# Kernel optimization log

Measured on AMD Instinct MI355X. Metric: run time of the kernel, lower is better.

Reference implementation:

```python
import jax, jax.numpy as jnp
import numpy as np
from jax import lax

INV_SQRT2 = np.float32(1.0 / np.sqrt(2.0))

def conv2d(x, w, b=None, stride=1, pad=0):
    y = lax.conv_general_dilated(x, w, (stride, stride), [(pad, pad), (pad, pad)],
                                 dimension_numbers=('NCHW', 'OIHW', 'NCHW'))
    return y if b is None else y + b[None, :, None, None]

def haar_dwt2_zero(x):
    # pytorch_wavelets DWTForward(J=1, wave='haar', mode='zero') for odd H,W:
    # pad one zero at the end of each spatial dim, then pairwise Haar analysis.
    x = jnp.pad(x, ((0, 0), (0, 0), (0, 1), (0, 1)))
    xe, xo = x[..., 0::2], x[..., 1::2]
    lo_w, hi_w = (xe + xo) * INV_SQRT2, (xe - xo) * INV_SQRT2
    def rows(t):
        te, to = t[:, :, 0::2, :], t[:, :, 1::2, :]
        return (te + to) * INV_SQRT2, (te - to) * INV_SQRT2
    ll, lh = rows(lo_w)
    hl, hh = rows(hi_w)
    return ll, lh, hl, hh  # cA, cH, cV, cD

def pixel_shuffle2(x):
    B, C, H, W = x.shape
    co = C // 4
    return x.reshape(B, co, 2, 2, H, W).transpose(0, 1, 4, 2, 5, 3).reshape(B, co, H * 2, W * 2)

def gaussian_kernel5(sigma=0.5):
    r = np.arange(5, dtype=np.float64) - 2.0
    k = np.exp(-(r ** 2) / (2.0 * sigma * sigma))
    return jnp.asarray((k / k.sum()).astype(np.float32))

_GK = gaussian_kernel5(0.5)

def gaussian_blur5(x4d):
    # cv2.GaussianBlur ksize=(5,5) sigma=0.5, default BORDER_REFLECT_101 -> 'reflect' pad
    p = jnp.pad(x4d, ((0, 0), (0, 0), (2, 2), (2, 2)), mode='reflect')
    p = conv2d(p, _GK.reshape(1, 1, 5, 1))
    return conv2d(p, _GK.reshape(1, 1, 1, 5))

def channel_attention(x, w1, w2):
    avg = jnp.mean(x, axis=(2, 3), keepdims=True)
    mx = jnp.max(x, axis=(2, 3), keepdims=True)
    mlp = lambda v: conv2d(jax.nn.relu(conv2d(v, w1)), w2)
    return jax.nn.sigmoid(mlp(avg) + mlp(mx)) * x

def _forward(x, w_x1, b_x1, w_x2, b_x2, w_x3, b_x3, w_hi, b_hi, w_lo, b_lo,
             ca1_w1, ca1_w2, ca2_w1, ca2_w2, w_cat, b_cat, w_c9a, b_c9a, w_c9b, b_c9b):
    f1 = jax.nn.relu(conv2d(x, w_x1, b_x1))            # (1,16,H,W)
    f2 = jax.nn.relu(conv2d(f1, w_x2, b_x2))           # (1,8,H,W)
    tmp12 = jax.nn.relu(conv2d(f2, w_x3, b_x3))        # (1,1,H,W)
    cA, cH, cV, cD = haar_dwt2_zero(tmp12)             # each (1,1,(H+1)/2,(W+1)/2)
    hf = pixel_shuffle2(jax.nn.relu(conv2d(jnp.concatenate([cH, cV, cD], 1), w_hi, b_hi, pad=1)))
    lf = pixel_shuffle2(jax.nn.relu(conv2d(cA, w_lo, b_lo, pad=1)))  # (1,1,H+5,W+5)
    # original detaches hf (cpu->numpy->cv2->cuda): gradients do not flow through it
    hf = gaussian_blur5(lax.stop_gradient(hf))
    hf = channel_attention(hf, ca1_w1, ca1_w2)
    lf = channel_attention(lf, ca2_w1, ca2_w2)
    alpha = 1.0
    cat = jax.nn.relu(conv2d(jnp.concatenate([alpha * hf, (1.0 - alpha) * lf], 1), w_cat, b_cat))
    f12 = tmp12 + cat                                   # (1,1,H,W)
    h = jax.nn.relu(conv2d(f12, w_c9a, b_c9a, pad=1))   # (1,32,H,W)
    return jax.nn.relu(conv2d(h, w_c9b, b_c9b, pad=1))  # (1,64,H,W)

def setup_inputs() -> dict:
    key = jax.random.key(0)
    ks = jax.random.split(key, 24)
    f32 = jnp.float32
    n = lambda k, s, sc=0.05: jax.random.normal(k, s, f32) * sc
    H = W = 511
    return {
        'x': jax.random.normal(ks[0], (1, 204, H, W), f32),
        'w_x1': n(ks[1], (16, 204, 1, 1)), 'b_x1': n(ks[2], (16,)),
        'w_x2': n(ks[3], (8, 16, 1, 1)),   'b_x2': n(ks[4], (8,)),
        'w_x3': n(ks[5], (1, 8, 1, 1)),    'b_x3': n(ks[6], (1,)),
        'w_hi': n(ks[7], (4, 3, 1, 1)),    'b_hi': n(ks[8], (4,)),
        'w_lo': n(ks[9], (4, 1, 1, 1)),    'b_lo': n(ks[10], (4,)),
        'ca1_w1': n(ks[11], (1, 1, 1, 1), 0.5), 'ca1_w2': n(ks[12], (1, 1, 1, 1), 0.5),
        'ca2_w1': n(ks[13], (1, 1, 1, 1), 0.5), 'ca2_w2': n(ks[14], (1, 1, 1, 1), 0.5),
        'w_cat': n(ks[15], (1, 2, 6, 6)),  'b_cat': n(ks[16], (1,)),
        'w_c9a': n(ks[17], (32, 1, 3, 3)), 'b_c9a': n(ks[18], (32,)),
        'w_c9b': n(ks[19], (64, 32, 3, 3)), 'b_c9b': n(ks[20], (64,)),
    }

def reference(x, w_x1, b_x1, w_x2, b_x2, w_x3, b_x3, w_hi, b_hi, w_lo, b_lo,
              ca1_w1, ca1_w2, ca2_w1, ca2_w2, w_cat, b_cat, w_c9a, b_c9a, w_c9b, b_c9b):
    return _forward(x, w_x1, b_x1, w_x2, b_x2, w_x3, b_x3, w_hi, b_hi, w_lo, b_lo,
                    ca1_w1, ca1_w2, ca2_w1, ca2_w2, w_cat, b_cat, w_c9a, b_c9a, w_c9b, b_c9b)
```

## Files before the change

kernel.cpp:

```cpp
#include <hip/hip_runtime.h>
#include <hip/hip_bf16.h>
#include <math.h>

#define NP    261121
#define WPX   520
#define ROWN  4160
#define PSTR  2138240
#define NBLUR 1041

typedef __attribute__((ext_vector_type(8))) short short8;
typedef __attribute__((ext_vector_type(4))) float f32x4;
typedef __attribute__((ext_vector_type(4), aligned(4))) float f32x4a;

static __device__ __forceinline__ unsigned short f2bf(float f) {
    unsigned int u = __builtin_bit_cast(unsigned int, f);
    u += 0x7FFFu + ((u >> 16) & 1u);
    return (unsigned short)(u >> 16);
}

static __device__ __forceinline__ short bf16s(float f) {
    __hip_bfloat16 h = __float2bfloat16(f);
    return __builtin_bit_cast(short, h);
}

__global__ __launch_bounds__(256, 4) void k_conv123(const float* __restrict__ x,
                                                    const float* __restrict__ w_x1,
                                                    const float* __restrict__ b1,
                                                    const float* __restrict__ w2,
                                                    const float* __restrict__ b2,
                                                    const float* __restrict__ w3,
                                                    const float* __restrict__ b3,
                                                    float* __restrict__ tmp12)
{
    int lane = threadIdx.x & 63, wave = threadIdx.x >> 6;
    int lpx = lane & 15, kg = lane >> 4;
    int s = blockIdx.x * 4 + wave;
    int pxb = s * 64;
    if (pxb > NP - 64) pxb = NP - 64;

    short8 afr[7];
    {
        const float* wrow = w_x1 + lpx * 204;
#pragma unroll
        for (int ks = 0; ks < 7; ++ks)
#pragma unroll
            for (int j = 0; j < 8; ++j) {
                int c = ks * 32 + kg * 8 + j;
                afr[ks][j] = (short)f2bf(c < 204 ? wrow[c] : 0.f);
            }
    }

    const float* pj[8];
#pragma unroll
    for (int j = 0; j < 8; ++j)
        pj[j] = x + (size_t)(kg * 8 + j) * NP + pxb + lpx * 4;

    f32x4 acc[4];
#pragma unroll
    for (int n = 0; n < 4; ++n) acc[n] = (f32x4){0.f, 0.f, 0.f, 0.f};

    f32x4a qA[8], qB[8];

#define LOADKS(Q, KS) do { \
        _Pragma("unroll") \
        for (int j = 0; j < 8; ++j) { \
            const size_t o = ((KS) < 6 || kg * 8 + j < 12) ? (size_t)(KS) * 32 * NP : 0; \
            Q[j] = *reinterpret_cast<const f32x4a*>(pj[j] + o); \
        } \
    } while (0)

#define PROC(Q, KS) do { \
        short8 bfr[4]; \
        _Pragma("unroll") \
        for (int n = 0; n < 4; ++n) \
            _Pragma("unroll") \
            for (int j = 0; j < 8; ++j) \
                bfr[n][j] = bf16s(Q[j][n]); \
        _Pragma("unroll") \
        for (int n = 0; n < 4; ++n) \
            acc[n] = __builtin_amdgcn_mfma_f32_16x16x32_bf16(afr[KS], bfr[n], acc[n], 0, 0, 0); \
    } while (0)

    LOADKS(qA, 0);
    LOADKS(qB, 1);
    PROC(qA, 0);
    LOADKS(qA, 2);
    PROC(qB, 1);
    LOADKS(qB, 3);
    PROC(qA, 2);
    LOADKS(qA, 4);
    PROC(qB, 3);
    LOADKS(qB, 5);
    PROC(qA, 4);
    LOADKS(qA, 6);
    PROC(qB, 5);
    PROC(qA, 6);
#undef LOADKS
#undef PROC

    float4 b1v = *reinterpret_cast<const float4*>(b1 + kg * 4);
    float4 w2v[8];
#pragma unroll
    for (int j = 0; j < 8; ++j)
        w2v[j] = *reinterpret_cast<const float4*>(w2 + j * 16 + kg * 4);
    float b2v[8], w3v[8];
#pragma unroll
    for (int j = 0; j < 8; ++j) { b2v[j] = b2[j]; w3v[j] = w3[j]; }
    float b3v = b3[0];

    f32x4 resv;
#pragma unroll
    for (int n = 0; n < 4; ++n) {
        float f0 = fmaxf(acc[n][0] + b1v.x, 0.f);
        float f1 = fmaxf(acc[n][1] + b1v.y, 0.f);
        float f2 = fmaxf(acc[n][2] + b1v.z, 0.f);
        float f3 = fmaxf(acc[n][3] + b1v.w, 0.f);
        float tmp = b3v;
#pragma unroll
        for (int j = 0; j < 8; ++j) {
            float sj = f0 * w2v[j].x;
            sj = fmaf(f1, w2v[j].y, sj);
            sj = fmaf(f2, w2v[j].z, sj);
            sj = fmaf(f3, w2v[j].w, sj);
            sj += __shfl_xor(sj, 16, 64);
            sj += __shfl_xor(sj, 32, 64);
            tmp = fmaf(fmaxf(sj + b2v[j], 0.f), w3v[j], tmp);
        }
        resv[n] = fmaxf(tmp, 0.f);
    }
    if (kg == 0)
        *reinterpret_cast<f32x4a*>(tmp12 + pxb + lpx * 4) = resv;
}

__global__ __launch_bounds__(256) void k_dwt(const float* __restrict__ tmp12,
                                             const float* __restrict__ w_hi,
                                             const float* __restrict__ b_hi,
                                             const float* __restrict__ w_c9b,
                                             float* __restrict__ hf,
                                             unsigned short* __restrict__ wb2,
                                             unsigned short* __restrict__ h2)
{
    int t = blockIdx.x * 256 + threadIdx.x;

    if (t < 18432) {
        int o = t / 288, ck = t - o * 288;
        int c = ck / 9, k = ck - c * 9;
        wb2[k * 2048 + o * 32 + c] = f2bf(w_c9b[t]);
    }
    short8 z8 = {0, 0, 0, 0, 0, 0, 0, 0};
    if (t < 4160) {
        int pl = t / 1040;
        int rr = t - pl * 1040;
        int row = rr >= 520 ? 512 : 0;
        int ch  = rr >= 520 ? rr - 520 : rr;
        *reinterpret_cast<short8*>(h2 + (size_t)pl * PSTR + (size_t)row * ROWN + ch * 8) = z8;
    }
    int z = t - 4160;
    if (z >= 0 && z < 6132) {
        int row = z / 12 + 1;
        int j = z - (row - 1) * 12;
        int pl = j / 3, cidx = j - pl * 3;
        int col = (cidx == 0) ? 0 : (cidx == 1 ? 512 : 513);
        *reinterpret_cast<short8*>(h2 + (size_t)pl * PSTR + (size_t)row * ROWN + col * 8) = z8;
    }

    const float INV = 0.70710678118654752440f;
    if (t >= 258 * 258) return;
    int h = t / 258, w = t - h * 258;

    float wh[12], bh[4];
#pragma unroll
    for (int i = 0; i < 12; ++i) wh[i] = w_hi[i];
#pragma unroll
    for (int o = 0; o < 4; ++o) bh[o] = b_hi[o];

    float v[4];
    if (h == 0 || h == 257 || w == 0 || w == 257) {
#pragma unroll
        for (int o = 0; o < 4; ++o) v[o] = fmaxf(bh[o], 0.f);
    } else {
        int hh = h - 1, ww = w - 1;
        int r0 = 2 * hh, r1 = 2 * hh + 1, c0 = 2 * ww, c1 = 2 * ww + 1;
        float a = tmp12[r0 * 511 + c0];
        float b = (c1 < 511) ? tmp12[r0 * 511 + c1] : 0.f;
        float c = (r1 < 511) ? tmp12[r1 * 511 + c0] : 0.f;
        float d = (r1 < 511 && c1 < 511) ? tmp12[r1 * 511 + c1] : 0.f;
        float lo0 = (a + b) * INV, hi0 = (a - b) * INV;
        float lo1 = (c + d) * INV, hi1 = (c - d) * INV;
        float cH = (lo0 - lo1) * INV;
        float cV = (hi0 + hi1) * INV;
        float cD = (hi0 - hi1) * INV;
#pragma unroll
        for (int o = 0; o < 4; ++o)
            v[o] = fmaxf(wh[o * 3 + 0] * cH + wh[o * 3 + 1] * cV + wh[o * 3 + 2] * cD + bh[o], 0.f);
    }
    int orow = (2 * h) * 516 + 2 * w;
    hf[orow]       = v[0];
    hf[orow + 1]   = v[1];
    hf[orow + 516] = v[2];
    hf[orow + 517] = v[3];
}

__global__ __launch_bounds__(256) void k_blur(const float* __restrict__ hf,
                                              float* __restrict__ hfb,
                                              float* __restrict__ psum,
                                              float* __restrict__ pmax,
                                              float g0, float g1, float g2)
{
    __shared__ float ss[256], sm[256];
    int t = threadIdx.x;
    int idx = blockIdx.x * 256 + t;
    bool ok = idx < 516 * 516;
    int idc = ok ? idx : 0;
    int y = idc / 516, x = idc - y * 516;
    float g[5] = {g0, g1, g2, g1, g0};
    int ry[5], rx[5];
#pragma unroll
    for (int i = 0; i < 5; ++i) {
        int yy = y + i - 2; yy = yy < 0 ? -yy : (yy > 515 ? 1030 - yy : yy);
        int xx = x + i - 2; xx = xx < 0 ? -xx : (xx > 515 ? 1030 - xx : xx);
        ry[i] = yy * 516; rx[i] = xx;
    }
    float s = 0.f;
#pragma unroll
    for (int i = 0; i < 5; ++i) {
        float rs = 0.f;
#pragma unroll
        for (int j = 0; j < 5; ++j) rs = fmaf(g[j], hf[ry[i] + rx[j]], rs);
        s = fmaf(g[i], rs, s);
    }
    if (ok) hfb[idx] = s;

    ss[t] = ok ? s : 0.f;
    sm[t] = ok ? s : -3.4e38f;
    __syncthreads();
    for (int off = 128; off > 0; off >>= 1) {
        if (t < off) { ss[t] += ss[t + off]; sm[t] = fmaxf(sm[t], sm[t + off]); }
        __syncthreads();
    }
    if (t == 0) { psum[blockIdx.x] = ss[0]; pmax[blockIdx.x] = sm[0]; }
}

__global__ __launch_bounds__(256) void k_cat(const float* __restrict__ hfb,
                                             const float* __restrict__ tmp12,
                                             const float* __restrict__ psum,
                                             const float* __restrict__ pmax,
                                             const float* __restrict__ caw1,
                                             const float* __restrict__ caw2,
                                             const float* __restrict__ w_cat,
                                             const float* __restrict__ b_cat,
                                             float* __restrict__ f12)
{
    __shared__ float ss[256], sm[256], ssc;
    int t = threadIdx.x;
    {
        float s = 0.f, m = -3.4e38f;
        for (int i = t; i < NBLUR; i += 256) { s += psum[i]; m = fmaxf(m, pmax[i]); }
        ss[t] = s; sm[t] = m;
        __syncthreads();
        for (int off = 128; off > 0; off >>= 1) {
            if (t < off) { ss[t] += ss[t + off]; sm[t] = fmaxf(sm[t], sm[t + off]); }
            __syncthreads();
        }
        if (t == 0) {
            float avg = ss[0] / 266256.f;
            float a = caw1[0], b = caw2[0];
            float z = b * fmaxf(a * avg, 0.f) + b * fmaxf(a * sm[0], 0.f);
            ssc = 1.f / (1.f + expf(-z));
        }
        __syncthreads();
    }
    float sc = ssc;

    int p = blockIdx.x * 256 + t;
    if (p >= NP) return;
    int y = p / 511, x = p - y * 511;
    float s = 0.f;
#pragma unroll
    for (int ky = 0; ky < 6; ++ky) {
        const float* row = hfb + (y + ky) * 516 + x;
#pragma unroll
        for (int kx = 0; kx < 6; ++kx) s = fmaf(row[kx], w_cat[ky * 6 + kx], s);
    }
    f12[p] = tmp12[p] + fmaxf(sc * s + b_cat[0], 0.f);
}

__global__ __launch_bounds__(256) void k_c9a(const float* __restrict__ f12,
                                             const float* __restrict__ w_c9a,
                                             const float* __restrict__ bias,
                                             unsigned short* __restrict__ h2)
{
    int p = blockIdx.x * 256 + threadIdx.x;
    if (p >= NP) return;
    int y = p / 511, x = p - y * 511;
    float hv[9];
#pragma unroll
    for (int ky = 0; ky < 3; ++ky)
#pragma unroll
        for (int kx = 0; kx < 3; ++kx) {
            int yy = y + ky - 1, xx = x + kx - 1;
            hv[ky * 3 + kx] = (yy >= 0 && yy < 511 && xx >= 0 && xx < 511) ? f12[yy * 511 + xx] : 0.f;
        }
    float acc[32];
#pragma unroll
    for (int o = 0; o < 32; ++o) acc[o] = bias[o];
#pragma unroll
    for (int k = 0; k < 9; ++k) {
        float v = hv[k];
#pragma unroll
        for (int o = 0; o < 32; ++o) acc[o] = fmaf(v, w_c9a[o * 9 + k], acc[o]);
    }
    unsigned short o16[32];
#pragma unroll
    for (int o = 0; o < 32; ++o) o16[o] = f2bf(fmaxf(acc[o], 0.f));
    size_t px = (size_t)(y + 1) * WPX + (x + 1);
#pragma unroll
    for (int i = 0; i < 4; ++i)
        *reinterpret_cast<short8*>(h2 + (size_t)i * PSTR + px * 8) =
            reinterpret_cast<const short8*>(o16)[i];
}

__global__ __launch_bounds__(256, 3) void k_c9b(const unsigned short* __restrict__ h2,
                                                const unsigned short* __restrict__ wb2,
                                                const float* __restrict__ bias,
                                                float* __restrict__ out)
{
    __shared__ unsigned short swu[9 * 2048];

    int bid = blockIdx.x;
    int xcd = bid & 7, jj = bid >> 3;
    const int q = 127, r = 6;
    int wg = (xcd < r ? xcd * (q + 1) : r * (q + 1) + (xcd - r) * q) + jj;

    int lane = threadIdx.x & 63;
    int wave = threadIdx.x >> 6;
    int y  = wg >> 1;
    int xh = wg & 1;
    int xb = xh * 256 + wave * 64;
    int lpx = lane & 15, kg = lane >> 4;

    {
        const short8* wsrc = reinterpret_cast<const short8*>(wb2);
        short8* wdst = reinterpret_cast<short8*>(swu);
        for (int d = threadIdx.x; d < 2304; d += 256) {
            int kt = d >> 8, rem = d & 255, m = rem >> 6, l = rem & 63;
            wdst[d] = wsrc[kt * 256 + (m * 16 + (l & 15)) * 4 + (l >> 4)];
        }
    }
    __syncthreads();

    f32x4 acc[4][4];
#pragma unroll
    for (int m = 0; m < 4; ++m)
#pragma unroll
        for (int n = 0; n < 4; ++n) acc[m][n] = (f32x4){0.f, 0.f, 0.f, 0.f};

    const unsigned short* hb = h2 + (size_t)kg * PSTR;
    const int base_px = (y + 1) * WPX + (xb + 1) + lpx;
    const int rowm = base_px - WPX, row0 = base_px, rowp = base_px + WPX;
    const short8* swv = reinterpret_cast<const short8*>(swu);

#define LOADB(BUF, ROW, DX) do { \
        const unsigned short* rp = hb + (size_t)((ROW) + (DX)) * 8; \
        BUF[0] = *reinterpret_cast<const short8*>(rp); \
        BUF[1] = *reinterpret_cast<const short8*>(rp + 128); \
        BUF[2] = *reinterpret_cast<const short8*>(rp + 256); \
        BUF[3] = *reinterpret_cast<const short8*>(rp + 384); \
    } while (0)

#define TAP(KT, BUF) do { \
        const short8* ap = swv + (KT) * 256 + lane; \
        short8 a0 = ap[0], a1 = ap[64], a2 = ap[128], a3 = ap[192]; \
        _Pragma("unroll") \
        for (int n = 0; n < 4; ++n) { \
            acc[0][n] = __builtin_amdgcn_mfma_f32_16x16x32_bf16(a0, BUF[n], acc[0][n], 0, 0, 0); \
            acc[1][n] = __builtin_amdgcn_mfma_f32_16x16x32_bf16(a1, BUF[n], acc[1][n], 0, 0, 0); \
            acc[2][n] = __builtin_amdgcn_mfma_f32_16x16x32_bf16(a2, BUF[n], acc[2][n], 0, 0, 0); \
            acc[3][n] = __builtin_amdgcn_mfma_f32_16x16x32_bf16(a3, BUF[n], acc[3][n], 0, 0, 0); \
        } \
    } while (0)

    short8 bX[4], bY[4], bZ[4];
    LOADB(bX, rowm, -1);
    LOADB(bY, rowm,  0);
    LOADB(bZ, rowm, +1); TAP(0, bX);
    LOADB(bX, row0, -1); TAP(1, bY);
    LOADB(bY, row0,  0); TAP(2, bZ);
    LOADB(bZ, row0, +1); TAP(3, bX);
    LOADB(bX, rowp, -1); TAP(4, bY);
    LOADB(bY, rowp,  0); TAP(5, bZ);
    LOADB(bZ, rowp, +1); TAP(6, bX);
    TAP(7, bY);
    TAP(8, bZ);
#undef LOADB
#undef TAP

    const int ybase = y * 511;
#pragma unroll
    for (int m = 0; m < 4; ++m) {
#pragma unroll
        for (int rr = 0; rr < 4; ++rr) {
            int o = m * 16 + kg * 4 + rr;
            float bo = bias[o];
#pragma unroll
            for (int n = 0; n < 4; ++n) {
                int px = xb + n * 16 + lpx;
                if (px < 511)
                    out[(size_t)o * NP + ybase + px] = fmaxf(acc[m][n][rr] + bo, 0.f);
            }
        }
    }
}

extern "C" void kernel_launch(void* const* d_in, const int* in_sizes, int n_in,
                              void* d_out, int out_size, void* d_ws, size_t ws_size,
                              hipStream_t stream)
{
    (void)in_sizes; (void)n_in; (void)out_size; (void)ws_size;

    const float* x     = (const float*)d_in[0];
    const float* w_x1  = (const float*)d_in[1];
    const float* b_x1  = (const float*)d_in[2];
    const float* w_x2  = (const float*)d_in[3];
    const float* b_x2  = (const float*)d_in[4];
    const float* w_x3  = (const float*)d_in[5];
    const float* b_x3  = (const float*)d_in[6];
    const float* w_hi  = (const float*)d_in[7];
    const float* b_hi  = (const float*)d_in[8];
    const float* ca1w1 = (const float*)d_in[11];
    const float* ca1w2 = (const float*)d_in[12];
    const float* w_cat = (const float*)d_in[15];
    const float* b_cat = (const float*)d_in[16];
    const float* w_c9a = (const float*)d_in[17];
    const float* b_c9a = (const float*)d_in[18];
    const float* w_c9b = (const float*)d_in[19];
    const float* b_c9b = (const float*)d_in[20];

    float* ws    = (float*)d_ws;
    float* tmp12 = ws + 0;
    float* hf    = ws + 261184;
    float* hfb   = ws + 527488;
    float* f12   = ws + 793792;
    float* psum  = ws + 1054976;
    float* pmax  = ws + 1056032;
    unsigned short* wb2 = (unsigned short*)(ws + 1057088);
    unsigned short* h2  = (unsigned short*)(ws + 1066304);

    float* out = (float*)d_out;

    double kk[5], ssum = 0.0;
    for (int i = 0; i < 5; ++i) { double r = i - 2.0; kk[i] = exp(-r * r / 0.5); ssum += kk[i]; }
    float g0 = (float)(kk[0] / ssum), g1 = (float)(kk[1] / ssum), g2 = (float)(kk[2] / ssum);

    k_conv123<<<1024, 256, 0, stream>>>(x, w_x1, b_x1, w_x2, b_x2, w_x3, b_x3, tmp12);
    k_dwt<<<261, 256, 0, stream>>>(tmp12, w_hi, b_hi, w_c9b, hf, wb2, h2);
    k_blur<<<NBLUR, 256, 0, stream>>>(hf, hfb, psum, pmax, g0, g1, g2);
    k_cat<<<1021, 256, 0, stream>>>(hfb, tmp12, psum, pmax, ca1w1, ca1w2, w_cat, b_cat, f12);
    k_c9a<<<1021, 256, 0, stream>>>(f12, w_c9a, b_c9a, h2);
    k_c9b<<<1022, 256, 0, stream>>>(h2, wb2, b_c9b, out);
}
```

Baseline: 125.4 us.

## Stage conv1 input through double-buffered LDS with wider per-block pixel tiles

The 204-channel 1x1 conv kernel now has each wave load 8 channel rows of 512 contiguous pixels, convert them to bf16 and write them into a double-buffered shared-memory tile. Waves then read the transposed MFMA B fragments from LDS, so each thread issues fewer and more coalesced global loads. Each block covers 512 pixels and each wave accumulates 8 MFMA tiles instead of 4, with half as many blocks launched. The cost is a __syncthreads per K-step, LDS traffic with possible bank conflicts, and lower occupancy (launch bounds 2).

```diff
diff --git a/kernel.cpp b/kernel.cpp
--- a/kernel.cpp
+++ b/kernel.cpp
@@ -3,12 +3,16 @@
 #include <math.h>
 
 #define NP    261121
+#define SPB   512
+#define RS    520
+#define OFS   16640
 #define WPX   520
 #define ROWN  4160
 #define PSTR  2138240
 #define NBLUR 1041
 
 typedef __attribute__((ext_vector_type(8))) short short8;
+typedef __attribute__((ext_vector_type(4))) short short4v;
 typedef __attribute__((ext_vector_type(4))) float f32x4;
 typedef __attribute__((ext_vector_type(4), aligned(4))) float f32x4a;
 
@@ -23,7 +27,7 @@
     return __builtin_bit_cast(short, h);
 }
 
-__global__ __launch_bounds__(256, 4) void k_conv123(const float* __restrict__ x,
+__global__ __launch_bounds__(256, 2) void k_conv123(const float* __restrict__ x,
                                                     const float* __restrict__ w_x1,
                                                     const float* __restrict__ b1,
                                                     const float* __restrict__ w2,
@@ -32,11 +36,13 @@
                                                     const float* __restrict__ b3,
                                                     float* __restrict__ tmp12)
 {
-    int lane = threadIdx.x & 63, wave = threadIdx.x >> 6;
-    int lpx = lane & 15, kg = lane >> 4;
-    int s = blockIdx.x * 4 + wave;
-    int pxb = s * 64;
-    if (pxb > NP - 64) pxb = NP - 64;
+    __shared__ unsigned short sb[2 * OFS];
+
+    const int tid = threadIdx.x;
+    const int v = tid >> 6, l = tid & 63;
+    const int lpx = l & 15, kg = l >> 4;
+    int pxb = blockIdx.x * SPB;
+    if (pxb > NP - SPB) pxb = NP - SPB;
 
     short8 afr[7];
     {
@@ -50,53 +56,74 @@
             }
     }
 
-    const float* pj[8];
-#pragma unroll
-    for (int j = 0; j < 8; ++j)
-        pj[j] = x + (size_t)(kg * 8 + j) * NP + pxb + lpx * 4;
-
-    f32x4 acc[4];
-#pragma unroll
-    for (int n = 0; n < 4; ++n) acc[n] = (f32x4){0.f, 0.f, 0.f, 0.f};
-
-    f32x4a qA[8], qB[8];
-
-#define LOADKS(Q, KS) do { \
+    const float* xb = x + pxb + 4 * l;
+    const float* lpB[8];
+#pragma unroll
+    for (int i = 0; i < 8; ++i)
+        lpB[i] = xb + (size_t)(v * 8 + i) * NP;
+
+    f32x4 acc[8];
+#pragma unroll
+    for (int n = 0; n < 8; ++n) acc[n] = (f32x4){0.f, 0.f, 0.f, 0.f};
+
+    f32x4a q0[8], q1[8];
+
+#define LOADISSUE(KS) do { \
         _Pragma("unroll") \
-        for (int j = 0; j < 8; ++j) { \
-            const size_t o = ((KS) < 6 || kg * 8 + j < 12) ? (size_t)(KS) * 32 * NP : 0; \
-            Q[j] = *reinterpret_cast<const f32x4a*>(pj[j] + o); \
+        for (int i = 0; i < 8; ++i) { \
+            const float* p = ((KS) < 6 || v * 8 + i < 12) ? lpB[i] + (size_t)(KS) * 32 * NP : xb; \
+            q0[i] = *reinterpret_cast<const f32x4a*>(p); \
+            q1[i] = *reinterpret_cast<const f32x4a*>(p + 256); \
         } \
     } while (0)
 
-#define PROC(Q, KS) do { \
-        short8 bfr[4]; \
+#define CVTWRITE(BUF) do { \
         _Pragma("unroll") \
-        for (int n = 0; n < 4; ++n) \
+        for (int i = 0; i < 8; ++i) { \
+            unsigned short* row = sb + (BUF) * OFS + (v * 8 + i) * RS; \
+            short4v w0, w1; \
             _Pragma("unroll") \
-            for (int j = 0; j < 8; ++j) \
-                bfr[n][j] = bf16s(Q[j][n]); \
+            for (int n = 0; n < 4; ++n) { w0[n] = bf16s(q0[i][n]); w1[n] = bf16s(q1[i][n]); } \
+            *reinterpret_cast<short4v*>(row + 4 * l)       = w0; \
+            *reinterpret_cast<short4v*>(row + 256 + 4 * l) = w1; \
+        } \
+    } while (0)
+
+#define COMPUTE(KS, BUF) do { \
+        short8 r0, r1, r2, r3, r4, r5, r6, r7; \
+        const unsigned short* base = sb + (BUF) * OFS + kg * 8 * RS + v * 128 + lpx * 8; \
+        r0 = *reinterpret_cast<const short8*>(base); \
+        r1 = *reinterpret_cast<const short8*>(base + RS); \
+        r2 = *reinterpret_cast<const short8*>(base + 2 * RS); \
+        r3 = *reinterpret_cast<const short8*>(base + 3 * RS); \
+        r4 = *reinterpret_cast<const short8*>(base + 4 * RS); \
+        r5 = *reinterpret_cast<const short8*>(base + 5 * RS); \
+        r6 = *reinterpret_cast<const short8*>(base + 6 * RS); \
+        r7 = *reinterpret_cast<const short8*>(base + 7 * RS); \
         _Pragma("unroll") \
-        for (int n = 0; n < 4; ++n) \
-            acc[n] = __builtin_amdgcn_mfma_f32_16x16x32_bf16(afr[KS], bfr[n], acc[n], 0, 0, 0); \
-    } while (0)
-
-    LOADKS(qA, 0);
-    LOADKS(qB, 1);
-    PROC(qA, 0);
-    LOADKS(qA, 2);
-    PROC(qB, 1);
-    LOADKS(qB, 3);
-    PROC(qA, 2);
-    LOADKS(qA, 4);
-    PROC(qB, 3);
-    LOADKS(qB, 5);
-    PROC(qA, 4);
-    LOADKS(qA, 6);
-    PROC(qB, 5);
-    PROC(qA, 6);
-#undef LOADKS
-#undef PROC
+        for (int n = 0; n < 8; ++n) { \
+            short8 b; \
+            b[0] = r0[n]; b[1] = r1[n]; b[2] = r2[n]; b[3] = r3[n]; \
+            b[4] = r4[n]; b[5] = r5[n]; b[6] = r6[n]; b[7] = r7[n]; \
+            acc[n] = __builtin_amdgcn_mfma_f32_16x16x32_bf16(afr[KS], b, acc[n], 0, 0, 0); \
+        } \
+    } while (0)
+
+    LOADISSUE(0);
+    CVTWRITE(0);
+
+#define STEP(K, LAST) do { \
+        if (!(LAST)) LOADISSUE((K) + 1); \
+        __syncthreads(); \
+        COMPUTE((K), (K) & 1); \
+        if (!(LAST)) CVTWRITE(((K) + 1) & 1); \
+    } while (0)
+
+    STEP(0, 0); STEP(1, 0); STEP(2, 0); STEP(3, 0); STEP(4, 0); STEP(5, 0); STEP(6, 1);
+#undef LOADISSUE
+#undef CVTWRITE
+#undef COMPUTE
+#undef STEP
 
     float4 b1v = *reinterpret_cast<const float4*>(b1 + kg * 4);
     float4 w2v[8];
@@ -108,9 +135,9 @@
     for (int j = 0; j < 8; ++j) { b2v[j] = b2[j]; w3v[j] = w3[j]; }
     float b3v = b3[0];
 
-    f32x4 resv;
-#pragma unroll
-    for (int n = 0; n < 4; ++n) {
+    f32x4 rlo, rhi;
+#pragma unroll
+    for (int n = 0; n < 8; ++n) {
         float f0 = fmaxf(acc[n][0] + b1v.x, 0.f);
         float f1 = fmaxf(acc[n][1] + b1v.y, 0.f);
         float f2 = fmaxf(acc[n][2] + b1v.z, 0.f);
@@ -126,10 +153,14 @@
             sj += __shfl_xor(sj, 32, 64);
             tmp = fmaf(fmaxf(sj + b2v[j], 0.f), w3v[j], tmp);
         }
-        resv[n] = fmaxf(tmp, 0.f);
-    }
-    if (kg == 0)
-        *reinterpret_cast<f32x4a*>(tmp12 + pxb + lpx * 4) = resv;
+        if (n < 4) rlo[n] = fmaxf(tmp, 0.f);
+        else       rhi[n - 4] = fmaxf(tmp, 0.f);
+    }
+    if (kg == 0) {
+        float* dst = tmp12 + pxb + v * 128 + lpx * 8;
+        *reinterpret_cast<f32x4a*>(dst)     = rlo;
+        *reinterpret_cast<f32x4a*>(dst + 4) = rhi;
+    }
 }
 
 __global__ __launch_bounds__(256) void k_dwt(const float* __restrict__ tmp12,
@@ -452,7 +483,7 @@
     for (int i = 0; i < 5; ++i) { double r = i - 2.0; kk[i] = exp(-r * r / 0.5); ssum += kk[i]; }
     float g0 = (float)(kk[0] / ssum), g1 = (float)(kk[1] / ssum), g2 = (float)(kk[2] / ssum);
 
-    k_conv123<<<1024, 256, 0, stream>>>(x, w_x1, b_x1, w_x2, b_x2, w_x3, b_x3, tmp12);
+    k_conv123<<<511, 256, 0, stream>>>(x, w_x1, b_x1, w_x2, b_x2, w_x3, b_x3, tmp12);
     k_dwt<<<261, 256, 0, stream>>>(tmp12, w_hi, b_hi, w_c9b, hf, wb2, h2);
     k_blur<<<NBLUR, 256, 0, stream>>>(hf, hfb, psum, pmax, g0, g1, g2);
     k_cat<<<1021, 256, 0, stream>>>(hfb, tmp12, psum, pmax, ca1w1, ca1w2, w_cat, b_cat, f12);
```

Result: faster. 113.0 us (-9.9%).

## Stage conv123 input through LDS with direct global-to-LDS async loads

Applied to the files above, without the earlier changes.

The 204-channel 1x1 conv kernel now streams each 32-channel slice of the input into a double-buffered shared-memory tile using global_load_lds, instead of each wave loading its own registers. A block covers 256 contiguous pixels, all waves cooperate on the staging, and a barrier separates stages. The aim is to make global reads fully coalesced and let loads overlap MFMA work while cutting register pressure. In exchange it adds 64KB of LDS per block, a lower occupancy hint, and a __syncthreads per stage.

```diff
diff --git a/kernel.cpp b/kernel.cpp
--- a/kernel.cpp
+++ b/kernel.cpp
@@ -3,6 +3,7 @@
 #include <math.h>
 
 #define NP    261121
+#define SPB   256
 #define WPX   520
 #define ROWN  4160
 #define PSTR  2138240
@@ -23,7 +24,14 @@
     return __builtin_bit_cast(short, h);
 }
 
-__global__ __launch_bounds__(256, 4) void k_conv123(const float* __restrict__ x,
+static __device__ __forceinline__ void gl_lds16(const float* g, float* l) {
+    __builtin_amdgcn_global_load_lds(
+        (const __attribute__((address_space(1))) unsigned int*)g,
+        (__attribute__((address_space(3))) unsigned int*)l,
+        16, 0, 0);
+}
+
+__global__ __launch_bounds__(256, 2) void k_conv123(const float* __restrict__ x,
                                                     const float* __restrict__ w_x1,
                                                     const float* __restrict__ b1,
                                                     const float* __restrict__ w2,
@@ -32,11 +40,13 @@
                                                     const float* __restrict__ b3,
                                                     float* __restrict__ tmp12)
 {
-    int lane = threadIdx.x & 63, wave = threadIdx.x >> 6;
-    int lpx = lane & 15, kg = lane >> 4;
-    int s = blockIdx.x * 4 + wave;
-    int pxb = s * 64;
-    if (pxb > NP - 64) pxb = NP - 64;
+    __shared__ float sb[2 * 32 * 256];
+
+    const int tid = threadIdx.x;
+    const int v = tid >> 6, l = tid & 63;
+    const int lpx = l & 15, kg = l >> 4;
+    int pxb = blockIdx.x * SPB;
+    if (pxb > NP - SPB) pxb = NP - SPB;
 
     short8 afr[7];
     {
@@ -50,53 +60,53 @@
             }
     }
 
-    const float* pj[8];
-#pragma unroll
-    for (int j = 0; j < 8; ++j)
-        pj[j] = x + (size_t)(kg * 8 + j) * NP + pxb + lpx * 4;
-
     f32x4 acc[4];
 #pragma unroll
     for (int n = 0; n < 4; ++n) acc[n] = (f32x4){0.f, 0.f, 0.f, 0.f};
 
-    f32x4a qA[8], qB[8];
-
-#define LOADKS(Q, KS) do { \
+#define STAGE(KS) do { \
         _Pragma("unroll") \
-        for (int j = 0; j < 8; ++j) { \
-            const size_t o = ((KS) < 6 || kg * 8 + j < 12) ? (size_t)(KS) * 32 * NP : 0; \
-            Q[j] = *reinterpret_cast<const f32x4a*>(pj[j] + o); \
+        for (int i = 0; i < 8; ++i) { \
+            const int ch = v * 8 + i; \
+            const float* src = ((KS) < 6 || ch < 12) \
+                ? x + (size_t)((KS) * 32 + ch) * NP + pxb + 4 * l \
+                : x + pxb + 4 * l;    \
+            gl_lds16(src, sb + ((KS) & 1) * 8192 + ch * 256); \
         } \
     } while (0)
 
-#define PROC(Q, KS) do { \
-        short8 bfr[4]; \
+#define COMPUTE(KS) do { \
+        const float* base = sb + ((KS) & 1) * 8192 + (kg * 8) * 256 + v * 64 + lpx * 4; \
+        f32x4 r0 = *reinterpret_cast<const f32x4*>(base); \
+        f32x4 r1 = *reinterpret_cast<const f32x4*>(base + 256); \
+        f32x4 r2 = *reinterpret_cast<const f32x4*>(base + 512); \
+        f32x4 r3 = *reinterpret_cast<const f32x4*>(base + 768); \
+        f32x4 r4 = *reinterpret_cast<const f32x4*>(base + 1024); \
+        f32x4 r5 = *reinterpret_cast<const f32x4*>(base + 1280); \
+        f32x4 r6 = *reinterpret_cast<const f32x4*>(base + 1536); \
+        f32x4 r7 = *reinterpret_cast<const f32x4*>(base + 1792); \
         _Pragma("unroll") \
-        for (int n = 0; n < 4; ++n) \
-            _Pragma("unroll") \
-            for (int j = 0; j < 8; ++j) \
-                bfr[n][j] = bf16s(Q[j][n]); \
-        _Pragma("unroll") \
-        for (int n = 0; n < 4; ++n) \
-            acc[n] = __builtin_amdgcn_mfma_f32_16x16x32_bf16(afr[KS], bfr[n], acc[n], 0, 0, 0); \
+        for (int n = 0; n < 4; ++n) { \
+            short8 b; \
+            b[0] = bf16s(r0[n]); b[1] = bf16s(r1[n]); \
+            b[2] = bf16s(r2[n]); b[3] = bf16s(r3[n]); \
+            b[4] = bf16s(r4[n]); b[5] = bf16s(r5[n]); \
+            b[6] = bf16s(r6[n]); b[7] = bf16s(r7[n]); \
+            acc[n] = __builtin_amdgcn_mfma_f32_16x16x32_bf16(afr[KS], b, acc[n], 0, 0, 0); \
+        } \
     } while (0)
 
-    LOADKS(qA, 0);
-    LOADKS(qB, 1);
-    PROC(qA, 0);
-    LOADKS(qA, 2);
-    PROC(qB, 1);
-    LOADKS(qB, 3);
-    PROC(qA, 2);
-    LOADKS(qA, 4);
-    PROC(qB, 3);
-    LOADKS(qB, 5);
-    PROC(qA, 4);
-    LOADKS(qA, 6);
-    PROC(qB, 5);
-    PROC(qA, 6);
-#undef LOADKS
-#undef PROC
+    STAGE(0);
+#define STEP(K, LAST) do { \
+        __syncthreads(); \
+        if (!(LAST)) STAGE((K) + 1); \
+        COMPUTE(K); \
+    } while (0)
+
+    STEP(0, 0); STEP(1, 0); STEP(2, 0); STEP(3, 0); STEP(4, 0); STEP(5, 0); STEP(6, 1);
+#undef STAGE
+#undef COMPUTE
+#undef STEP
 
     float4 b1v = *reinterpret_cast<const float4*>(b1 + kg * 4);
     float4 w2v[8];
@@ -129,7 +139,7 @@
         resv[n] = fmaxf(tmp, 0.f);
     }
     if (kg == 0)
-        *reinterpret_cast<f32x4a*>(tmp12 + pxb + lpx * 4) = resv;
+        *reinterpret_cast<f32x4a*>(tmp12 + pxb + v * 64 + lpx * 4) = resv;
 }
 
 __global__ __launch_bounds__(256) void k_dwt(const float* __restrict__ tmp12,
@@ -452,7 +462,7 @@
     for (int i = 0; i < 5; ++i) { double r = i - 2.0; kk[i] = exp(-r * r / 0.5); ssum += kk[i]; }
     float g0 = (float)(kk[0] / ssum), g1 = (float)(kk[1] / ssum), g2 = (float)(kk[2] / ssum);
 
-    k_conv123<<<1024, 256, 0, stream>>>(x, w_x1, b_x1, w_x2, b_x2, w_x3, b_x3, tmp12);
+    k_conv123<<<1021, 256, 0, stream>>>(x, w_x1, b_x1, w_x2, b_x2, w_x3, b_x3, tmp12);
     k_dwt<<<261, 256, 0, stream>>>(tmp12, w_hi, b_hi, w_c9b, hf, wb2, h2);
     k_blur<<<NBLUR, 256, 0, stream>>>(hf, hfb, psum, pmax, g0, g1, g2);
     k_cat<<<1021, 256, 0, stream>>>(hfb, tmp12, psum, pmax, ca1w1, ca1w2, w_cat, b_cat, f12);
```

New measurement: 117.1 us. -6.6%, faster.
